# Optimization experiments

Hardware: AMD Instinct MI355X
Metric: run time of the kernel (lower is better)

Reference implementation:

```python
import jax, jax.numpy as jnp
import numpy as np

B, N, NEMBED, E, H = 4, 256, 10000, 63, 128
D = E + 1  # feature dim after concat = 64


def _lin(key, fan_in, fan_out):
    k1, k2 = jax.random.split(key)
    bound = 1.0 / np.sqrt(fan_in)
    W = jax.random.uniform(k1, (fan_in, fan_out), jnp.float32, -bound, bound)
    b = jax.random.uniform(k2, (fan_out,), jnp.float32, -bound, bound)
    return W, b


def setup_inputs() -> dict:
    key = jax.random.key(0)
    ks = jax.random.split(key, 9)
    xcat = jax.random.randint(ks[0], (B, N), 0, NEMBED, dtype=jnp.int64)
    xfeat = jax.random.normal(ks[1], (B, N), dtype=jnp.float32)
    emb = jax.random.normal(ks[2], (NEMBED, E), dtype=jnp.float32)
    W1, b1 = _lin(ks[3], D, H)
    W2, b2 = _lin(ks[4], H, H)
    W3, b3 = _lin(ks[5], H, H)
    D1, c1 = _lin(ks[6], H, H)
    D2, c2 = _lin(ks[7], H, H)
    D3, c3 = _lin(ks[8], H, 1)
    return {"xcat": xcat, "xfeat": xfeat, "emb": emb,
            "W1": W1, "b1": b1, "W2": W2, "b2": b2, "W3": W3, "b3": b3,
            "D1": D1, "c1": c1, "D2": D2, "c2": c2, "D3": D3, "c3": c3}


def reference(xcat, xfeat, emb, W1, b1, W2, b2, W3, b3, D1, c1, D2, c2, D3, c3):
    # embed + concat scalar feature -> [B, N, D]
    x = jnp.concatenate([emb[xcat], xfeat[..., None]], axis=-1)
    # pairwise outer product over the set dim -> [B, N, N, D]
    # (original: einsum 'bid,bjd->bdij' then permute(0,2,3,1) == 'bid,bjd->bijd')
    p = jnp.einsum('bid,bjd->bijd', x, x)
    # per-pair 3-layer MLP (enc)
    h = jnp.maximum(p @ W1 + b1, 0.0)
    h = jnp.maximum(h @ W2 + b2, 0.0)
    h = h @ W3 + b3
    # relu -> mean pool over (i, j) -> relu; dropout is identity in eval
    h = jnp.maximum(h, 0.0)
    h = jnp.mean(h, axis=(1, 2))  # [B, H]
    h = jnp.maximum(h, 0.0)
    # dec MLP -> [B, 1]
    h = jnp.maximum(h @ D1 + c1, 0.0)
    h = jnp.maximum(h @ D2 + c2, 0.0)
    return h @ D3 + c3
```

## Files before the change

kernel.cpp:

```cpp
#include <hip/hip_runtime.h>


#define NB 4
#define NN 256
#define HD 128
#define TPB 257
#define NPAIR 32896

typedef _Float16 half_t;
typedef __attribute__((ext_vector_type(8))) _Float16 half8;
typedef __attribute__((ext_vector_type(4))) float f32x4;

__device__ __forceinline__ unsigned pkrtz(float a, float b) {
    return __builtin_bit_cast(unsigned, __builtin_amdgcn_cvt_pkrtz(a, b));
}

__device__ __forceinline__ void tri_ij(int t, int& i, int& j) {
    j = (int)((sqrtf(8.0f * (float)t + 1.0f) - 1.0f) * 0.5f);
    while (((j + 1) * (j + 2) >> 1) <= t) ++j;
    while (((j * (j + 1)) >> 1) > t) --j;
    i = t - ((j * (j + 1)) >> 1);
}

__device__ __forceinline__ void pack_w(const float* __restrict__ W, half_t* __restrict__ pw,
                                       int KQ, int u) {
    int l  = u & 63;
    int kq = (u >> 6) % KQ;
    int mt = (u >> 6) / KQ;
    int q = l >> 4, m = l & 15;
    int c = mt * 16 + m;
#pragma unroll
    for (int j = 0; j < 8; ++j) {
        int k = kq * 32 + q * 8 + j;
        pw[u * 8 + j] = (half_t)W[k * 128 + c];
    }
}

__global__ void prep_kernel(const int* __restrict__ xcat,
                            const float* __restrict__ xfeat,
                            const float* __restrict__ emb,
                            const float* __restrict__ W1,
                            const float* __restrict__ W2,
                            const float* __restrict__ W3,
                            half_t* __restrict__ x,
                            half_t* __restrict__ pw1,
                            half_t* __restrict__ pw2,
                            half_t* __restrict__ pw3,
                            unsigned short* __restrict__ lut)
{
    int bid = blockIdx.x;
    int tid = threadIdx.x;
    if (bid < 256) {
        int f = bid * 256 + tid;
        int d = f & 63;
        int nn = f >> 6;
        float v;
        if (d < 63) v = emb[xcat[nn] * 63 + d];
        else        v = xfeat[nn];
        x[f] = (half_t)v;
    } else if (bid < 260) {
        pack_w(W1, pw1, 2, (bid - 256) * 256 + tid);
    } else if (bid < 268) {
        pack_w(W2, pw2, 4, (bid - 260) * 256 + tid);
    } else if (bid < 276) {
        pack_w(W3, pw3, 4, (bid - 268) * 256 + tid);
    } else {
        int t = (bid - 276) * 256 + tid;
        if (t < NPAIR) {
            int i, j;
            tri_ij(t, i, j);
            lut[t] = (unsigned short)(i | (j << 8));
        }
    }
}

__global__ __launch_bounds__(256, 3) void pair_mlp(
    const half_t* __restrict__ x,
    const unsigned short* __restrict__ lut,
    const half_t* __restrict__ pw1, const float* __restrict__ b1,
    const half_t* __restrict__ pw2, const float* __restrict__ b2,
    const half_t* __restrict__ pw3, const float* __restrict__ b3,
    float* __restrict__ partialOut)
{
    __shared__ half_t smP[128 * 64];
    __shared__ half_t smH[128 * 128];
    __shared__ float smW[128];

    const int tid = threadIdx.x;
    const int l = tid & 63;
    const int w = __builtin_amdgcn_readfirstlane(tid >> 6);
    const int wm = w >> 1;
    const int wn = w & 1;
    const int q = l >> 4;
    const int m = l & 15;
    const int b = blockIdx.y;
    const int tbase = blockIdx.x * 128;
    const half_t* xb = x + (b << 14);
    char* smPc = (char*)smP;
    char* smHc = (char*)smH;

    {
        const int p = tid >> 1;
        const int hf = tid & 1;
        unsigned short ij = lut[tbase + p];
        int i = ij & 255, j = ij >> 8;
        if (hf == 0) smW[p] = (i == j) ? 1.0f : 2.0f;
        const half8* xi = (const half8*)(xb + (i << 6) + hf * 32);
        const half8* xj = (const half8*)(xb + (j << 6) + hf * 32);
#pragma unroll
        for (int c = 0; c < 4; ++c) {
            half8 s = xi[c] * xj[c];
            int chunk = hf * 4 + c;
            int phys = chunk ^ (p & 7);
            *(uint4*)(smPc + p * 128 + phys * 16) = __builtin_bit_cast(uint4, s);
        }
    }
    __syncthreads();

    f32x4 acc[4][4];

#pragma unroll
    for (int mt = 0; mt < 4; ++mt) {
        float4 bv = *(const float4*)(b1 + (wm * 4 + mt) * 16 + q * 4);
        f32x4 init = {bv.x, bv.y, bv.z, bv.w};
#pragma unroll
        for (int nt = 0; nt < 4; ++nt) acc[mt][nt] = init;
    }

#pragma unroll
    for (int kq = 0; kq < 2; ++kq) {
        half8 bfr[4], afr[4];
#pragma unroll
        for (int nt = 0; nt < 4; ++nt) {
            int pair = wn * 64 + nt * 16 + m;
            int phys = (kq * 4 + q) ^ (pair & 7);
            bfr[nt] = *(const half8*)(smPc + pair * 128 + phys * 16);
        }
#pragma unroll
        for (int mt = 0; mt < 4; ++mt)
            afr[mt] = *(const half8*)(pw1 + ((((wm * 4 + mt) * 2 + kq) * 64 + l) << 3));
#pragma unroll
        for (int mt = 0; mt < 4; ++mt)
#pragma unroll
            for (int nt = 0; nt < 4; ++nt)
                acc[mt][nt] = __builtin_amdgcn_mfma_f32_16x16x32_f16(afr[mt], bfr[nt], acc[mt][nt], 0, 0, 0);
    }

#pragma unroll
    for (int mt = 0; mt < 4; ++mt) {
        int mtg = wm * 4 + mt;
#pragma unroll
        for (int nt = 0; nt < 4; ++nt) {
            int pair = wn * 64 + nt * 16 + m;
            uint2 sv;
            sv.x = pkrtz(fmaxf(acc[mt][nt][0], 0.f), fmaxf(acc[mt][nt][1], 0.f));
            sv.y = pkrtz(fmaxf(acc[mt][nt][2], 0.f), fmaxf(acc[mt][nt][3], 0.f));
            int chunk = mtg * 2 + (q >> 1);
            int phys = chunk ^ (pair & 15);
            *(uint2*)(smHc + pair * 256 + phys * 16 + (q & 1) * 8) = sv;
        }
    }
    __syncthreads();

#pragma unroll
    for (int mt = 0; mt < 4; ++mt) {
        float4 bv = *(const float4*)(b2 + (wm * 4 + mt) * 16 + q * 4);
        f32x4 init = {bv.x, bv.y, bv.z, bv.w};
#pragma unroll
        for (int nt = 0; nt < 4; ++nt) acc[mt][nt] = init;
    }

#pragma unroll
    for (int kq = 0; kq < 4; ++kq) {
        half8 bfr[4], afr[4];
#pragma unroll
        for (int nt = 0; nt < 4; ++nt) {
            int pair = wn * 64 + nt * 16 + m;
            int phys = (kq * 4 + q) ^ (pair & 15);
            bfr[nt] = *(const half8*)(smHc + pair * 256 + phys * 16);
        }
#pragma unroll
        for (int mt = 0; mt < 4; ++mt)
            afr[mt] = *(const half8*)(pw2 + ((((wm * 4 + mt) * 4 + kq) * 64 + l) << 3));
#pragma unroll
        for (int mt = 0; mt < 4; ++mt)
#pragma unroll
            for (int nt = 0; nt < 4; ++nt)
                acc[mt][nt] = __builtin_amdgcn_mfma_f32_16x16x32_f16(afr[mt], bfr[nt], acc[mt][nt], 0, 0, 0);
    }
    __syncthreads();

#pragma unroll
    for (int mt = 0; mt < 4; ++mt) {
        int mtg = wm * 4 + mt;
#pragma unroll
        for (int nt = 0; nt < 4; ++nt) {
            int pair = wn * 64 + nt * 16 + m;
            uint2 sv;
            sv.x = pkrtz(fmaxf(acc[mt][nt][0], 0.f), fmaxf(acc[mt][nt][1], 0.f));
            sv.y = pkrtz(fmaxf(acc[mt][nt][2], 0.f), fmaxf(acc[mt][nt][3], 0.f));
            int chunk = mtg * 2 + (q >> 1);
            int phys = chunk ^ (pair & 15);
            *(uint2*)(smHc + pair * 256 + phys * 16 + (q & 1) * 8) = sv;
        }
    }
    __syncthreads();

#pragma unroll
    for (int mt = 0; mt < 4; ++mt) {
        float4 bv = *(const float4*)(b3 + (wm * 4 + mt) * 16 + q * 4);
        f32x4 init = {bv.x, bv.y, bv.z, bv.w};
#pragma unroll
        for (int nt = 0; nt < 4; ++nt) acc[mt][nt] = init;
    }

#pragma unroll
    for (int kq = 0; kq < 4; ++kq) {
        half8 bfr[4], afr[4];
#pragma unroll
        for (int nt = 0; nt < 4; ++nt) {
            int pair = wn * 64 + nt * 16 + m;
            int phys = (kq * 4 + q) ^ (pair & 15);
            bfr[nt] = *(const half8*)(smHc + pair * 256 + phys * 16);
        }
#pragma unroll
        for (int mt = 0; mt < 4; ++mt)
            afr[mt] = *(const half8*)(pw3 + ((((wm * 4 + mt) * 4 + kq) * 64 + l) << 3));
#pragma unroll
        for (int mt = 0; mt < 4; ++mt)
#pragma unroll
            for (int nt = 0; nt < 4; ++nt)
                acc[mt][nt] = __builtin_amdgcn_mfma_f32_16x16x32_f16(afr[mt], bfr[nt], acc[mt][nt], 0, 0, 0);
    }

    float wpv[4];
#pragma unroll
    for (int nt = 0; nt < 4; ++nt)
        wpv[nt] = smW[wn * 64 + nt * 16 + m];

    float* smPart = (float*)smP;
#pragma unroll
    for (int mt = 0; mt < 4; ++mt) {
        int mtg = wm * 4 + mt;
        float vs[4];
#pragma unroll
        for (int r = 0; r < 4; ++r) {
            vs[r] = wpv[0] * fmaxf(acc[mt][0][r], 0.f) + wpv[1] * fmaxf(acc[mt][1][r], 0.f)
                  + wpv[2] * fmaxf(acc[mt][2][r], 0.f) + wpv[3] * fmaxf(acc[mt][3][r], 0.f);
#pragma unroll
            for (int s = 1; s < 16; s <<= 1)
                vs[r] += __shfl_xor(vs[r], s, 64);
        }
        if (m == 0) {
            float* p = smPart + wn * HD + mtg * 16 + q * 4;
            p[0] = vs[0]; p[1] = vs[1]; p[2] = vs[2]; p[3] = vs[3];
        }
    }
    __syncthreads();

    if (tid < HD) {
        float v = smPart[tid] + smPart[HD + tid];
        partialOut[(b * TPB + blockIdx.x) * HD + tid] = v;
    }
}

__global__ __launch_bounds__(1024) void reduce_decode(
    const float* __restrict__ partial,
    const float* __restrict__ D1, const float* __restrict__ c1,
    const float* __restrict__ D2, const float* __restrict__ c2,
    const float* __restrict__ D3, const float* __restrict__ c3,
    float* __restrict__ out)
{
    __shared__ float red8[8][HD];
    __shared__ float red2[2][HD];
    __shared__ float hb[HD];
    __shared__ float tb[HD];
    const int b = blockIdx.x;
    const int t = threadIdx.x;
    const int ch = t & 127, sl = t >> 7;

    {
        const float* base = partial + b * TPB * HD + ch;
        float s0 = 0.f, s1 = 0.f, s2 = 0.f, s3 = 0.f;
        int tl = sl;
        for (; tl + 32 <= TPB; tl += 32) {
            s0 += base[(tl     ) * HD];
            s1 += base[(tl +  8) * HD];
            s2 += base[(tl + 16) * HD];
            s3 += base[(tl + 24) * HD];
        }
        for (; tl < TPB; tl += 8) s0 += base[tl * HD];
        red8[sl][ch] = (s0 + s1) + (s2 + s3);
    }
    __syncthreads();
    if (sl == 0) {
        float v = ((red8[0][ch] + red8[1][ch]) + (red8[2][ch] + red8[3][ch]))
                + ((red8[4][ch] + red8[5][ch]) + (red8[6][ch] + red8[7][ch]));
        hb[ch] = fmaxf(v * (1.0f / 65536.0f), 0.0f);
    }
    __syncthreads();

    const int hf = sl & 1;

    if (t < 256) {
        float a = 0.f;
        for (int k = hf * 64; k < hf * 64 + 64; ++k)
            a = fmaf(hb[k], D1[(k << 7) + ch], a);
        red2[hf][ch] = a;
    }
    __syncthreads();
    if (t < 128)
        tb[ch] = fmaxf(red2[0][ch] + red2[1][ch] + c1[ch], 0.0f);
    __syncthreads();

    if (t < 256) {
        float a = 0.f;
        for (int k = hf * 64; k < hf * 64 + 64; ++k)
            a = fmaf(tb[k], D2[(k << 7) + ch], a);
        red2[hf][ch] = a;
    }
    __syncthreads();
    if (t < 128)
        hb[ch] = fmaxf(red2[0][ch] + red2[1][ch] + c2[ch], 0.0f);
    __syncthreads();

    if (t < 128) red2[0][ch] = hb[ch] * D3[ch];
    __syncthreads();
    if (t < 64) {
        float r = red2[0][t] + red2[0][t + 64];
#pragma unroll
        for (int s2 = 1; s2 < 64; s2 <<= 1)
            r += __shfl_xor(r, s2, 64);
        if (t == 0) out[b] = r + c3[0];
    }
}

extern "C" void kernel_launch(void* const* d_in, const int* in_sizes, int n_in,
                              void* d_out, int out_size, void* d_ws, size_t ws_size,
                              hipStream_t stream)
{
    (void)in_sizes; (void)n_in; (void)out_size; (void)ws_size;

    const int*   xcat  = (const int*)  d_in[0];
    const float* xfeat = (const float*)d_in[1];
    const float* emb   = (const float*)d_in[2];
    const float* W1    = (const float*)d_in[3];
    const float* b1    = (const float*)d_in[4];
    const float* W2    = (const float*)d_in[5];
    const float* b2    = (const float*)d_in[6];
    const float* W3    = (const float*)d_in[7];
    const float* b3    = (const float*)d_in[8];
    const float* D1    = (const float*)d_in[9];
    const float* c1    = (const float*)d_in[10];
    const float* D2    = (const float*)d_in[11];
    const float* c2    = (const float*)d_in[12];
    const float* D3    = (const float*)d_in[13];
    const float* c3    = (const float*)d_in[14];
    float* out = (float*)d_out;

    half_t* x   = (half_t*)d_ws;
    half_t* pw1 = x + NB * NN * 64;
    half_t* pw2 = pw1 + 8 * 2 * 64 * 8;
    half_t* pw3 = pw2 + 8 * 4 * 64 * 8;
    unsigned short* lut = (unsigned short*)(pw3 + 8 * 4 * 64 * 8);
    float* partial = (float*)(lut + NPAIR);

    prep_kernel<<<405, 256, 0, stream>>>(xcat, xfeat, emb, W1, W2, W3,
                                         x, pw1, pw2, pw3, lut);
    pair_mlp<<<dim3(TPB, NB), 256, 0, stream>>>(x, lut, pw1, b1, pw2, b2, pw3, b3, partial);
    reduce_decode<<<NB, 1024, 0, stream>>>(partial, D1, c1, D2, c2, D3, c3, out);
}
```

Baseline: 109.4 us.

## Fuse reduce/decode into pair MLP via last-block atomic ticket

Removes the separate reduce_decode launch. Each pair_mlp block fences its partial sums and increments a per-batch ticket, and the last block to arrive does the cross-block reduction and the decoder MLP using 256 threads instead of 1024. This saves one kernel launch and its gap, but adds a threadfence and atomic to every block and leaves the tail reduction with fewer threads. The tickets are reset in prep_kernel on every call.

```diff
diff --git a/kernel.cpp b/kernel.cpp
--- a/kernel.cpp
+++ b/kernel.cpp
@@ -46,7 +46,8 @@
                             half_t* __restrict__ pw1,
                             half_t* __restrict__ pw2,
                             half_t* __restrict__ pw3,
-                            unsigned short* __restrict__ lut)
+                            unsigned short* __restrict__ lut,
+                            int* __restrict__ ticket)
 {
     int bid = blockIdx.x;
     int tid = threadIdx.x;
@@ -71,6 +72,7 @@
             tri_ij(t, i, j);
             lut[t] = (unsigned short)(i | (j << 8));
         }
+        if (bid == 276 && tid < NB) ticket[tid] = 0;
     }
 }
 
@@ -80,11 +82,17 @@
     const half_t* __restrict__ pw1, const float* __restrict__ b1,
     const half_t* __restrict__ pw2, const float* __restrict__ b2,
     const half_t* __restrict__ pw3, const float* __restrict__ b3,
-    float* __restrict__ partialOut)
+    float* __restrict__ partialOut,
+    int* __restrict__ ticket,
+    const float* __restrict__ D1, const float* __restrict__ c1,
+    const float* __restrict__ D2, const float* __restrict__ c2,
+    const float* __restrict__ D3, const float* __restrict__ c3,
+    float* __restrict__ out)
 {
     __shared__ half_t smP[128 * 64];
     __shared__ half_t smH[128 * 128];
     __shared__ float smW[128];
+    __shared__ int isLast;
 
     const int tid = threadIdx.x;
     const int l = tid & 63;
@@ -262,76 +270,69 @@
         float v = smPart[tid] + smPart[HD + tid];
         partialOut[(b * TPB + blockIdx.x) * HD + tid] = v;
     }
-}
-
-__global__ __launch_bounds__(1024) void reduce_decode(
-    const float* __restrict__ partial,
-    const float* __restrict__ D1, const float* __restrict__ c1,
-    const float* __restrict__ D2, const float* __restrict__ c2,
-    const float* __restrict__ D3, const float* __restrict__ c3,
-    float* __restrict__ out)
-{
-    __shared__ float red8[8][HD];
-    __shared__ float red2[2][HD];
-    __shared__ float hb[HD];
-    __shared__ float tb[HD];
-    const int b = blockIdx.x;
-    const int t = threadIdx.x;
-    const int ch = t & 127, sl = t >> 7;
+
+    __threadfence();
+    __syncthreads();
+    if (tid == 0)
+        isLast = (atomicAdd(&ticket[b], 1) == TPB - 1);
+    __syncthreads();
+    if (!isLast) return;
+    __threadfence();
+
+    float* redA = (float*)smP;
+    float* hb   = redA + 2 * HD;
+    float* tb   = hb + HD;
+    float* red2 = tb + HD;
+    const int ch = tid & 127, sl = tid >> 7;
 
     {
-        const float* base = partial + b * TPB * HD + ch;
+        const float* basep = partialOut + b * TPB * HD + ch;
         float s0 = 0.f, s1 = 0.f, s2 = 0.f, s3 = 0.f;
         int tl = sl;
-        for (; tl + 32 <= TPB; tl += 32) {
-            s0 += base[(tl     ) * HD];
-            s1 += base[(tl +  8) * HD];
-            s2 += base[(tl + 16) * HD];
-            s3 += base[(tl + 24) * HD];
-        }
-        for (; tl < TPB; tl += 8) s0 += base[tl * HD];
-        red8[sl][ch] = (s0 + s1) + (s2 + s3);
-    }
-    __syncthreads();
-    if (sl == 0) {
-        float v = ((red8[0][ch] + red8[1][ch]) + (red8[2][ch] + red8[3][ch]))
-                + ((red8[4][ch] + red8[5][ch]) + (red8[6][ch] + red8[7][ch]));
-        hb[ch] = fmaxf(v * (1.0f / 65536.0f), 0.0f);
-    }
-    __syncthreads();
-
-    const int hf = sl & 1;
-
-    if (t < 256) {
+        for (; tl + 8 <= TPB; tl += 8) {
+            s0 += basep[(tl    ) * HD];
+            s1 += basep[(tl + 2) * HD];
+            s2 += basep[(tl + 4) * HD];
+            s3 += basep[(tl + 6) * HD];
+        }
+        for (; tl < TPB; tl += 2) s0 += basep[tl * HD];
+        redA[sl * HD + ch] = (s0 + s1) + (s2 + s3);
+    }
+    __syncthreads();
+    if (sl == 0)
+        hb[ch] = fmaxf((redA[ch] + redA[HD + ch]) * (1.0f / 65536.0f), 0.0f);
+    __syncthreads();
+
+    {
         float a = 0.f;
-        for (int k = hf * 64; k < hf * 64 + 64; ++k)
+        for (int k = sl * 64; k < sl * 64 + 64; ++k)
             a = fmaf(hb[k], D1[(k << 7) + ch], a);
-        red2[hf][ch] = a;
-    }
-    __syncthreads();
-    if (t < 128)
-        tb[ch] = fmaxf(red2[0][ch] + red2[1][ch] + c1[ch], 0.0f);
-    __syncthreads();
-
-    if (t < 256) {
+        red2[sl * HD + ch] = a;
+    }
+    __syncthreads();
+    if (sl == 0)
+        tb[ch] = fmaxf(red2[ch] + red2[HD + ch] + c1[ch], 0.0f);
+    __syncthreads();
+
+    {
         float a = 0.f;
-        for (int k = hf * 64; k < hf * 64 + 64; ++k)
+        for (int k = sl * 64; k < sl * 64 + 64; ++k)
             a = fmaf(tb[k], D2[(k << 7) + ch], a);
-        red2[hf][ch] = a;
-    }
-    __syncthreads();
-    if (t < 128)
-        hb[ch] = fmaxf(red2[0][ch] + red2[1][ch] + c2[ch], 0.0f);
-    __syncthreads();
-
-    if (t < 128) red2[0][ch] = hb[ch] * D3[ch];
-    __syncthreads();
-    if (t < 64) {
-        float r = red2[0][t] + red2[0][t + 64];
-#pragma unroll
-        for (int s2 = 1; s2 < 64; s2 <<= 1)
-            r += __shfl_xor(r, s2, 64);
-        if (t == 0) out[b] = r + c3[0];
+        red2[sl * HD + ch] = a;
+    }
+    __syncthreads();
+    if (sl == 0)
+        hb[ch] = fmaxf(red2[ch] + red2[HD + ch] + c2[ch], 0.0f);
+    __syncthreads();
+
+    if (sl == 0) red2[ch] = hb[ch] * D3[ch];
+    __syncthreads();
+    if (tid < 64) {
+        float r = red2[tid] + red2[tid + 64];
+#pragma unroll
+        for (int sv = 1; sv < 64; sv <<= 1)
+            r += __shfl_xor(r, sv, 64);
+        if (tid == 0) out[b] = r + c3[0];
     }
 }
 
@@ -364,9 +365,11 @@
     half_t* pw3 = pw2 + 8 * 4 * 64 * 8;
     unsigned short* lut = (unsigned short*)(pw3 + 8 * 4 * 64 * 8);
     float* partial = (float*)(lut + NPAIR);
+    int* ticket = (int*)(partial + NB * TPB * HD);
 
     prep_kernel<<<405, 256, 0, stream>>>(xcat, xfeat, emb, W1, W2, W3,
-                                         x, pw1, pw2, pw3, lut);
-    pair_mlp<<<dim3(TPB, NB), 256, 0, stream>>>(x, lut, pw1, b1, pw2, b2, pw3, b3, partial);
-    reduce_decode<<<NB, 1024, 0, stream>>>(partial, D1, c1, D2, c2, D3, c3, out);
-}
+                                         x, pw1, pw2, pw3, lut, ticket);
+    pair_mlp<<<dim3(TPB, NB), 256, 0, stream>>>(x, lut, pw1, b1, pw2, b2, pw3, b3,
+                                                partial, ticket,
+                                                D1, c1, D2, c2, D3, c3, out);
+}
```

Result: slower. 179.1 us (+63.6%).
